# Performance work log

Measured on AMD Instinct MI355X. Metric: run time of the kernel, lower is better.

## Reference

```python
import jax, jax.numpy as jnp
import numpy as np

N = 65536  # number of 3D query points
H = 60     # hidden width


def setup_inputs() -> dict:
    key = jax.random.key(0)
    ks = jax.random.split(key, 11)
    return {
        "x": jax.random.normal(ks[0], (N, 3), jnp.float32),
        "w1": jax.random.normal(ks[1], (H, 3), jnp.float32) * 0.5,
        "b1": jax.random.normal(ks[2], (H,), jnp.float32) * 0.1,
        "w2": jax.random.normal(ks[3], (H, H), jnp.float32) * 0.13,
        "b2": jax.random.normal(ks[4], (H,), jnp.float32) * 0.1,
        "w3": jax.random.normal(ks[5], (H, H), jnp.float32) * 0.13,
        "b3": jax.random.normal(ks[6], (H,), jnp.float32) * 0.1,
        "w4": jax.random.normal(ks[7], (H, H), jnp.float32) * 0.13,
        "b4": jax.random.normal(ks[8], (H,), jnp.float32) * 0.1,
        "w5": jax.random.normal(ks[9], (1, H), jnp.float32) * 0.13,
        "b5": jax.random.normal(ks[10], (1,), jnp.float32) * 0.1,
    }


def reference(x, w1, b1, w2, b2, w3, b3, w4, b4, w5, b5):
    # Batched version of the per-point ChairMLP forward.
    # neuron_state(x, W, b) builds diag(s) @ [W|b] with s = (relu_out != 0);
    # diag(s) @ W == W * s[:, None], so the whole thing is a row mask.
    # wl_k = W_k.T * s_k (cols masked), bias_k = b_k * s_k.
    # Chained products P_k = wl1 @ ... @ wl_k and B_k = affine bias chain are
    # computed without materializing [N,60,60] per-sample matrices:
    #   P_k = (P_{k-1} @ W_k.T) * s_k = alk_k_w * s_k
    #   B_k = (B_{k-1} @ W_k.T + b_k) * s_k = alk_k_b * s_k
    n = x.shape[0]
    dt = x.dtype

    h1 = jax.nn.relu(x @ w1.T + b1)                      # [N,60]
    s1 = (h1 > 0).astype(dt)
    P1 = w1.T[None, :, :] * s1[:, None, :]               # [N,3,60]
    B1 = b1 * s1                                          # [N,60]
    alk1 = jnp.broadcast_to(
        jnp.concatenate([w1.T, b1[None, :]], axis=0), (n, 4, H))

    h2 = jax.nn.relu(h1 @ w2.T + b2)
    s2 = (h2 > 0).astype(dt)
    alk2_w = jnp.einsum('nij,kj->nik', P1, w2)           # [N,3,60]
    alk2_b = B1 @ w2.T + b2                              # [N,60]
    alk2 = jnp.concatenate([alk2_w, alk2_b[:, None, :]], axis=1)
    P2 = alk2_w * s2[:, None, :]
    B2 = alk2_b * s2

    h3 = jax.nn.relu(h2 @ w3.T + b3)
    s3 = (h3 > 0).astype(dt)
    alk3_w = jnp.einsum('nij,kj->nik', P2, w3)
    alk3_b = B2 @ w3.T + b3
    alk3 = jnp.concatenate([alk3_w, alk3_b[:, None, :]], axis=1)
    P3 = alk3_w * s3[:, None, :]
    B3 = alk3_b * s3

    h4 = jax.nn.relu(h3 @ w4.T + b4)
    s4 = (h4 > 0).astype(dt)
    alk4_w = jnp.einsum('nij,kj->nik', P3, w4)
    alk4_b = B3 @ w4.T + b4
    alk4 = jnp.concatenate([alk4_w, alk4_b[:, None, :]], axis=1)
    P4 = alk4_w * s4[:, None, :]
    B4 = alk4_b * s4

    out = h4 @ w5.T + b5                                  # [N,1]
    zs_w = jnp.einsum('nij,kj->nik', P4, w5)             # [N,3,1]
    zs_b = B4 @ w5.T + b5                                 # [N,1]
    zerosurface = jnp.concatenate([zs_w, zs_b[:, None, :]], axis=1)  # [N,4,1]

    S = jnp.stack([s1, s2, s3, s4], axis=1)               # [N,4,60] == S.t() per sample
    return out, S, alk1, alk2, alk3, alk4, zerosurface
```

## Files before the change

### kernel.cpp

```cpp
#include <hip/hip_runtime.h>


constexpr int  NP = 65536;
constexpr int  HD = 60;
constexpr long CH = (long)NP * 4 * HD;
constexpr long OFF_OUT  = 0;
constexpr long OFF_S    = NP;
constexpr long OFF_ALK1 = OFF_S + CH;
constexpr long OFF_ZS   = OFF_ALK1 + 4 * CH;

__global__ __launch_bounds__(256, 3) void chair_fused(
    const float* __restrict__ x,
    const float* __restrict__ w1, const float* __restrict__ b1,
    const float* __restrict__ w2, const float* __restrict__ b2,
    const float* __restrict__ w3, const float* __restrict__ b3,
    const float* __restrict__ w4, const float* __restrict__ b4,
    const float* __restrict__ w5, const float* __restrict__ b5,
    float* __restrict__ out)
{
    __shared__ float hb[2][64][68];

    const int tid = threadIdx.x;
    const int lp  = tid >> 2;
    const int r   = tid & 3;
    const int n   = blockIdx.x * 64 + lp;
    const long t  = (long)n * 4 + r;
    const bool isb = (r == 3);
    float* Sp = out + OFF_S + (long)n * (4 * HD);

    const float x0 = x[3*n+0], x1 = x[3*n+1], x2 = x[3*n+2];
#pragma unroll
    for (int jj = 0; jj < 15; ++jj) {
        const int j = 4*jj + r;
        float acc = b1[j];
        acc = fmaf(x0, w1[3*j+0], acc);
        acc = fmaf(x1, w1[3*j+1], acc);
        acc = fmaf(x2, w1[3*j+2], acc);
        Sp[j] = acc > 0.f ? 1.f : 0.f;
        hb[1][lp][j] = acc > 0.f ? acc : 0.f;
    }
    __syncthreads();

    float row[60];
    {
        float* alkp = out + OFF_ALK1 + t * HD;
#pragma unroll
        for (int c0 = 0; c0 < 60; c0 += 4) {
            float4 wv;
            wv.x = isb ? b1[c0+0] : w1[3*(c0+0) + r];
            wv.y = isb ? b1[c0+1] : w1[3*(c0+1) + r];
            wv.z = isb ? b1[c0+2] : w1[3*(c0+2) + r];
            wv.w = isb ? b1[c0+3] : w1[3*(c0+3) + r];
            *reinterpret_cast<float4*>(alkp + c0) = wv;
            float4 hp = *reinterpret_cast<const float4*>(&hb[1][lp][c0]);
            row[c0+0] = hp.x > 0.f ? wv.x : 0.f;
            row[c0+1] = hp.y > 0.f ? wv.y : 0.f;
            row[c0+2] = hp.z > 0.f ? wv.z : 0.f;
            row[c0+3] = hp.w > 0.f ? wv.w : 0.f;
        }
    }

    float zacc = isb ? b5[0] : 0.f;

#pragma unroll 1
    for (int k = 2; k <= 4; ++k) {
        const float* __restrict__ W = (k == 2) ? w2 : ((k == 3) ? w3 : w4);
        const float* __restrict__ B = (k == 2) ? b2 : ((k == 3) ? b3 : b4);
        const int bc = k & 1;
        const int bp = (k - 1) & 1;

        {
            float h[60];
#pragma unroll
            for (int c0 = 0; c0 < 60; c0 += 4)
                *reinterpret_cast<float4*>(&h[c0]) =
                    *reinterpret_cast<const float4*>(&hb[bp][lp][c0]);
            float* Sk = Sp + (k-1) * HD;
#pragma unroll 1
            for (int jj = 0; jj < 15; ++jj) {
                const int j = 4*jj + r;
                const float* wr = W + j * HD;
                float a0 = B[j], a1 = 0.f, a2 = 0.f, a3 = 0.f;
#pragma unroll
                for (int q = 0; q < 15; q += 4) {
                    {
                        float4 wv = *reinterpret_cast<const float4*>(wr + 4*q);
                        a0 = fmaf(h[4*q+0], wv.x, a0); a0 = fmaf(h[4*q+1], wv.y, a0);
                        a0 = fmaf(h[4*q+2], wv.z, a0); a0 = fmaf(h[4*q+3], wv.w, a0);
                    }
                    if (q + 1 < 15) {
                        float4 wv = *reinterpret_cast<const float4*>(wr + 4*(q+1));
                        a1 = fmaf(h[4*q+4], wv.x, a1); a1 = fmaf(h[4*q+5], wv.y, a1);
                        a1 = fmaf(h[4*q+6], wv.z, a1); a1 = fmaf(h[4*q+7], wv.w, a1);
                    }
                    if (q + 2 < 15) {
                        float4 wv = *reinterpret_cast<const float4*>(wr + 4*(q+2));
                        a2 = fmaf(h[4*q+8],  wv.x, a2); a2 = fmaf(h[4*q+9],  wv.y, a2);
                        a2 = fmaf(h[4*q+10], wv.z, a2); a2 = fmaf(h[4*q+11], wv.w, a2);
                    }
                    if (q + 3 < 15) {
                        float4 wv = *reinterpret_cast<const float4*>(wr + 4*(q+3));
                        a3 = fmaf(h[4*q+12], wv.x, a3); a3 = fmaf(h[4*q+13], wv.y, a3);
                        a3 = fmaf(h[4*q+14], wv.z, a3); a3 = fmaf(h[4*q+15], wv.w, a3);
                    }
                }
                float acc = (a0 + a1) + (a2 + a3);
                Sk[j] = acc > 0.f ? 1.f : 0.f;
                hb[bc][lp][j] = acc > 0.f ? acc : 0.f;
            }
        }
        __syncthreads();

        {
            float nrow[60];
            float* alkc = out + OFF_ALK1 + (long)(k-1) * CH + t * HD;
#pragma unroll 1
            for (int j0 = 0; j0 < 60; j0 += 12) {
                float acc[12];
#pragma unroll
                for (int jj = 0; jj < 12; ++jj) acc[jj] = isb ? B[j0+jj] : 0.f;
#pragma unroll
                for (int jj = 0; jj < 12; ++jj) {
                    const float* wr = W + (j0+jj) * HD;
#pragma unroll
                    for (int c = 0; c < 60; ++c)
                        acc[jj] = fmaf(row[c], wr[c], acc[jj]);
                }
#pragma unroll
                for (int jj = 0; jj < 12; jj += 4) {
                    float4 v = { acc[jj], acc[jj+1], acc[jj+2], acc[jj+3] };
                    *reinterpret_cast<float4*>(alkc + j0 + jj) = v;
                }
#pragma unroll
                for (int jj = 0; jj < 12; ++jj) nrow[j0+jj] = acc[jj];
            }
#pragma unroll
            for (int c0 = 0; c0 < 60; c0 += 4) {
                float4 hp = *reinterpret_cast<const float4*>(&hb[bc][lp][c0]);
                row[c0+0] = hp.x > 0.f ? nrow[c0+0] : 0.f;
                row[c0+1] = hp.y > 0.f ? nrow[c0+1] : 0.f;
                row[c0+2] = hp.z > 0.f ? nrow[c0+2] : 0.f;
                row[c0+3] = hp.w > 0.f ? nrow[c0+3] : 0.f;
            }
        }
        if (k == 4) {
#pragma unroll
            for (int c = 0; c < 60; ++c)
                zacc = fmaf(row[c], w5[c], zacc);
        }
    }

    out[OFF_ZS + t] = zacc;

    if (r == 0) {
        float acc = b5[0];
#pragma unroll
        for (int c0 = 0; c0 < 60; c0 += 4) {
            float4 hv = *reinterpret_cast<const float4*>(&hb[0][lp][c0]);
            float4 wv = *reinterpret_cast<const float4*>(w5 + c0);
            acc = fmaf(hv.x, wv.x, acc);
            acc = fmaf(hv.y, wv.y, acc);
            acc = fmaf(hv.z, wv.z, acc);
            acc = fmaf(hv.w, wv.w, acc);
        }
        out[OFF_OUT + n] = acc;
    }
}

extern "C" void kernel_launch(void* const* d_in, const int* in_sizes, int n_in,
                              void* d_out, int out_size, void* d_ws, size_t ws_size,
                              hipStream_t stream) {
    const float* x  = (const float*)d_in[0];
    const float* w1 = (const float*)d_in[1];
    const float* b1 = (const float*)d_in[2];
    const float* w2 = (const float*)d_in[3];
    const float* b2 = (const float*)d_in[4];
    const float* w3 = (const float*)d_in[5];
    const float* b3 = (const float*)d_in[6];
    const float* w4 = (const float*)d_in[7];
    const float* b4 = (const float*)d_in[8];
    const float* w5 = (const float*)d_in[9];
    const float* b5 = (const float*)d_in[10];
    float* out = (float*)d_out;

    chair_fused<<<NP / 64, 256, 0, stream>>>(
        x, w1, b1, w2, b2, w3, b3, w4, b4, w5, b5, out);
}
```

Measured before the change: 726.2 us.

## Stage layer weight matrices in LDS and fully unroll the hidden and alk loops

Each block now copies the current 60x60 weight matrix into shared memory, with barriers before and after, and both the hidden-activation matvec and the alk row matvec read weights from LDS instead of global memory. The previous loops were kept rolled and split across four partial accumulators; they are now fully unrolled over a single accumulator per output. The aim is to cut repeated global or scalar-cache weight loads. In exchange the kernel adds LDS traffic, extra syncs per layer, and more register pressure from full unrolling under the launch bound of 3 blocks per CU.

```diff
diff --git a/kernel.cpp b/kernel.cpp
--- a/kernel.cpp
+++ b/kernel.cpp
@@ -18,6 +18,7 @@
     const float* __restrict__ w5, const float* __restrict__ b5,
     float* __restrict__ out)
 {
+    __shared__ float Wl[HD * HD];
     __shared__ float hb[2][64][68];
 
     const int tid = threadIdx.x;
@@ -32,20 +33,20 @@
 #pragma unroll
     for (int jj = 0; jj < 15; ++jj) {
         const int j = 4*jj + r;
-        float acc = b1[j];
-        acc = fmaf(x0, w1[3*j+0], acc);
-        acc = fmaf(x1, w1[3*j+1], acc);
-        acc = fmaf(x2, w1[3*j+2], acc);
-        Sp[j] = acc > 0.f ? 1.f : 0.f;
-        hb[1][lp][j] = acc > 0.f ? acc : 0.f;
+        float pre = b1[j];
+        pre = fmaf(x0, w1[3*j+0], pre);
+        pre = fmaf(x1, w1[3*j+1], pre);
+        pre = fmaf(x2, w1[3*j+2], pre);
+        Sp[j] = pre > 0.f ? 1.f : 0.f;
+        hb[1][lp][j] = pre > 0.f ? pre : 0.f;
     }
     __syncthreads();
 
-    float row[60];
+    float row[HD];
     {
         float* alkp = out + OFF_ALK1 + t * HD;
 #pragma unroll
-        for (int c0 = 0; c0 < 60; c0 += 4) {
+        for (int c0 = 0; c0 < HD; c0 += 4) {
             float4 wv;
             wv.x = isb ? b1[c0+0] : w1[3*(c0+0) + r];
             wv.y = isb ? b1[c0+1] : w1[3*(c0+1) + r];
@@ -69,42 +70,39 @@
         const int bc = k & 1;
         const int bp = (k - 1) & 1;
 
+        __syncthreads();
+
         {
-            float h[60];
+            const float4* Wg = reinterpret_cast<const float4*>(W);
+            float4* Ws = reinterpret_cast<float4*>(Wl);
 #pragma unroll
-            for (int c0 = 0; c0 < 60; c0 += 4)
+            for (int it = 0; it < 4; ++it) {
+                int iw = tid + 256 * it;
+                if (iw < 900) Ws[iw] = Wg[iw];
+            }
+        }
+        __syncthreads();
+
+        {
+            float h[HD];
+#pragma unroll
+            for (int c0 = 0; c0 < HD; c0 += 4)
                 *reinterpret_cast<float4*>(&h[c0]) =
                     *reinterpret_cast<const float4*>(&hb[bp][lp][c0]);
             float* Sk = Sp + (k-1) * HD;
-#pragma unroll 1
+#pragma unroll
             for (int jj = 0; jj < 15; ++jj) {
                 const int j = 4*jj + r;
-                const float* wr = W + j * HD;
-                float a0 = B[j], a1 = 0.f, a2 = 0.f, a3 = 0.f;
+                const float* wr = &Wl[j * HD];
+                float acc = B[j];
 #pragma unroll
-                for (int q = 0; q < 15; q += 4) {
-                    {
-                        float4 wv = *reinterpret_cast<const float4*>(wr + 4*q);
-                        a0 = fmaf(h[4*q+0], wv.x, a0); a0 = fmaf(h[4*q+1], wv.y, a0);
-                        a0 = fmaf(h[4*q+2], wv.z, a0); a0 = fmaf(h[4*q+3], wv.w, a0);
-                    }
-                    if (q + 1 < 15) {
-                        float4 wv = *reinterpret_cast<const float4*>(wr + 4*(q+1));
-                        a1 = fmaf(h[4*q+4], wv.x, a1); a1 = fmaf(h[4*q+5], wv.y, a1);
-                        a1 = fmaf(h[4*q+6], wv.z, a1); a1 = fmaf(h[4*q+7], wv.w, a1);
-                    }
-                    if (q + 2 < 15) {
-                        float4 wv = *reinterpret_cast<const float4*>(wr + 4*(q+2));
-                        a2 = fmaf(h[4*q+8],  wv.x, a2); a2 = fmaf(h[4*q+9],  wv.y, a2);
-                        a2 = fmaf(h[4*q+10], wv.z, a2); a2 = fmaf(h[4*q+11], wv.w, a2);
-                    }
-                    if (q + 3 < 15) {
-                        float4 wv = *reinterpret_cast<const float4*>(wr + 4*(q+3));
-                        a3 = fmaf(h[4*q+12], wv.x, a3); a3 = fmaf(h[4*q+13], wv.y, a3);
-                        a3 = fmaf(h[4*q+14], wv.z, a3); a3 = fmaf(h[4*q+15], wv.w, a3);
-                    }
+                for (int c0 = 0; c0 < HD; c0 += 4) {
+                    float4 wv = *reinterpret_cast<const float4*>(wr + c0);
+                    acc = fmaf(h[c0+0], wv.x, acc);
+                    acc = fmaf(h[c0+1], wv.y, acc);
+                    acc = fmaf(h[c0+2], wv.z, acc);
+                    acc = fmaf(h[c0+3], wv.w, acc);
                 }
-                float acc = (a0 + a1) + (a2 + a3);
                 Sk[j] = acc > 0.f ? 1.f : 0.f;
                 hb[bc][lp][j] = acc > 0.f ? acc : 0.f;
             }
@@ -112,19 +110,24 @@
         __syncthreads();
 
         {
-            float nrow[60];
+            float nrow[HD];
             float* alkc = out + OFF_ALK1 + (long)(k-1) * CH + t * HD;
-#pragma unroll 1
-            for (int j0 = 0; j0 < 60; j0 += 12) {
+#pragma unroll
+            for (int j0 = 0; j0 < HD; j0 += 12) {
                 float acc[12];
 #pragma unroll
                 for (int jj = 0; jj < 12; ++jj) acc[jj] = isb ? B[j0+jj] : 0.f;
 #pragma unroll
                 for (int jj = 0; jj < 12; ++jj) {
-                    const float* wr = W + (j0+jj) * HD;
+                    const float* wr = &Wl[(j0+jj) * HD];
 #pragma unroll
-                    for (int c = 0; c < 60; ++c)
-                        acc[jj] = fmaf(row[c], wr[c], acc[jj]);
+                    for (int c0 = 0; c0 < HD; c0 += 4) {
+                        float4 wv = *reinterpret_cast<const float4*>(wr + c0);
+                        acc[jj] = fmaf(row[c0+0], wv.x, acc[jj]);
+                        acc[jj] = fmaf(row[c0+1], wv.y, acc[jj]);
+                        acc[jj] = fmaf(row[c0+2], wv.z, acc[jj]);
+                        acc[jj] = fmaf(row[c0+3], wv.w, acc[jj]);
+                    }
                 }
 #pragma unroll
                 for (int jj = 0; jj < 12; jj += 4) {
@@ -135,7 +138,7 @@
                 for (int jj = 0; jj < 12; ++jj) nrow[j0+jj] = acc[jj];
             }
 #pragma unroll
-            for (int c0 = 0; c0 < 60; c0 += 4) {
+            for (int c0 = 0; c0 < HD; c0 += 4) {
                 float4 hp = *reinterpret_cast<const float4*>(&hb[bc][lp][c0]);
                 row[c0+0] = hp.x > 0.f ? nrow[c0+0] : 0.f;
                 row[c0+1] = hp.y > 0.f ? nrow[c0+1] : 0.f;
@@ -145,7 +148,7 @@
         }
         if (k == 4) {
 #pragma unroll
-            for (int c = 0; c < 60; ++c)
+            for (int c = 0; c < HD; ++c)
                 zacc = fmaf(row[c], w5[c], zacc);
         }
     }
@@ -155,7 +158,7 @@
     if (r == 0) {
         float acc = b5[0];
 #pragma unroll
-        for (int c0 = 0; c0 < 60; c0 += 4) {
+        for (int c0 = 0; c0 < HD; c0 += 4) {
             float4 hv = *reinterpret_cast<const float4*>(&hb[0][lp][c0]);
             float4 wv = *reinterpret_cast<const float4*>(w5 + c0);
             acc = fmaf(hv.x, wv.x, acc);
```

Result: slower. 871.6 us (+20.0%).
